# Optimization experiments

Measured on AMD Instinct MI355X. Metric: run time of the kernel, lower is better.

## Reference

```python
import jax, jax.numpy as jnp
import numpy as np

N = 100000
E = 1600000
IN_CH = 128
HID = 128
HEADS = 4
C = HID // HEADS  # 32 per-head channels
NUM_CLASSES = 40
NEG_SLOPE = 0.2


def _glorot(key, shape):
    fan_in, fan_out = shape[0], shape[-1]
    lim = jnp.sqrt(6.0 / (fan_in + fan_out))
    return jax.random.uniform(key, shape, jnp.float32, -lim, lim)


def setup_inputs() -> dict:
    key = jax.random.key(0)
    ks = jax.random.split(key, 12)
    x = jax.random.normal(ks[0], (N, IN_CH), jnp.float32)
    edge_index = jax.random.randint(ks[1], (2, E), 0, N, jnp.int64)
    edge_weight = jax.random.uniform(ks[2], (E,), jnp.float32)
    return {
        'x': x,
        'edge_index': edge_index,
        'edge_weight': edge_weight,
        'W_pre': _glorot(ks[3], (IN_CH, HID)),
        'Wl': _glorot(ks[4], (HID, HEADS * C)),
        'bl': jnp.zeros((HEADS * C,), jnp.float32),
        'Wr': _glorot(ks[5], (HID, HEADS * C)),
        'br': jnp.zeros((HEADS * C,), jnp.float32),
        'We': _glorot(ks[6], (1, HEADS * C)),
        'att': _glorot(ks[7], (HEADS, C)),
        'b_gat': jnp.zeros((HEADS * C,), jnp.float32),
        'W1': _glorot(ks[8], (HID, HID)),
        'b1': jnp.zeros((HID,), jnp.float32),
        'W2': _glorot(ks[9], (HID, NUM_CLASSES)),
        'b2': jnp.zeros((NUM_CLASSES,), jnp.float32),
    }


def reference(x, edge_index, edge_weight, W_pre, Wl, bl, Wr, br, We, att, b_gat, W1, b1, W2, b2):
    # pre projection (bias=False), norm = Identity
    h0 = x @ W_pre  # [N, HID]

    # --- GATv2Conv (PyG semantics, eval mode) ---
    # add self loops; self-loop edge_attr = mean of existing edge_attr (fill_value='mean')
    loop = jnp.arange(N, dtype=edge_index.dtype)
    src = jnp.concatenate([edge_index[0], loop])  # [E+N]
    dst = jnp.concatenate([edge_index[1], loop])
    ea = jnp.concatenate([edge_weight, jnp.full((N,), jnp.mean(edge_weight), edge_weight.dtype)])  # [E+N]

    x_l = (h0 @ Wl + bl).reshape(N, HEADS, C)  # source transform
    x_r = (h0 @ Wr + br).reshape(N, HEADS, C)  # target transform
    edge_emb = (ea[:, None] * We).reshape(-1, HEADS, C)  # lin_edge (bias=False)

    xj = x_l[src]  # [Etot, H, C] gather of source features
    e = jax.nn.leaky_relu(xj + x_r[dst] + edge_emb, NEG_SLOPE)
    alpha = jnp.einsum('ehc,hc->eh', e, att)  # [Etot, H]

    # segment softmax over destination neighborhoods
    amax = jax.ops.segment_max(alpha, dst, num_segments=N)
    amax = jnp.where(jnp.isfinite(amax), amax, 0.0)
    ex = jnp.exp(alpha - amax[dst])
    denom = jax.ops.segment_sum(ex, dst, num_segments=N)
    attn = ex / (denom[dst] + 1e-16)  # [Etot, H]

    out = jax.ops.segment_sum(attn[:, :, None] * xj, dst, num_segments=N)  # [N, H, C]
    out = out.reshape(N, HEADS * C) + b_gat

    h1 = jax.nn.elu(out)
    h = h0 + h1  # residual

    logits = jax.nn.relu(h @ W1 + b1) @ W2 + b2
    return h, logits
```

## Files before the change

### kernel.cpp

```cpp
#include <hip/hip_runtime.h>

typedef __attribute__((ext_vector_type(8))) short short8;
typedef __attribute__((ext_vector_type(16))) float f32x16;

#if __has_builtin(__builtin_amdgcn_exp2f)
#define EXP2(x) __builtin_amdgcn_exp2f(x)
#else
#define EXP2(x) exp2f(x)
#endif

static __device__ __forceinline__ unsigned short f2bf(float f){
  unsigned u = __float_as_uint(f);
  unsigned r = u + 0x7fffu + ((u >> 16) & 1u);
  return (unsigned short)(r >> 16);
}
static __device__ __forceinline__ float bf2f(unsigned short h){
  return __uint_as_float(((unsigned)h) << 16);
}

__global__ void wprep(const float* __restrict__ Wpre, const float* __restrict__ Wl,
                      const float* __restrict__ Wr, const float* __restrict__ W1,
                      const float* __restrict__ W2, const float* __restrict__ bl,
                      const float* __restrict__ br,
                      unsigned short* __restrict__ Phi, unsigned short* __restrict__ Plo,
                      unsigned short* __restrict__ Lhi, unsigned short* __restrict__ Llo,
                      unsigned short* __restrict__ W1hi, unsigned short* __restrict__ W1lo,
                      unsigned short* __restrict__ W2hi, unsigned short* __restrict__ W2lo,
                      float* __restrict__ bcat){
  int i = blockIdx.x*256 + threadIdx.x;
  float v; unsigned short* hp; unsigned short* lp; int oi;
  if (i < 16384){
    int c = i >> 7, k = i & 127;
    v = Wpre[(size_t)k*128 + c]; hp = Phi; lp = Plo; oi = i;
  } else if (i < 49152){
    int j = i - 16384; int c = j >> 7, k = j & 127;
    v = (c < 128) ? Wl[(size_t)k*128 + c] : Wr[(size_t)k*128 + (c-128)];
    hp = Lhi; lp = Llo; oi = j;
  } else if (i < 65536){
    int j = i - 49152; int c = j >> 7, k = j & 127;
    v = W1[(size_t)k*128 + c]; hp = W1hi; lp = W1lo; oi = j;
  } else if (i < 70656){
    int j = i - 65536; int c = j >> 7, k = j & 127;
    v = W2[(size_t)k*40 + c]; hp = W2hi; lp = W2lo; oi = j;
  } else if (i < 70912){
    int j = i - 70656;
    bcat[j] = (j < 128) ? bl[j] : br[j-128];
    return;
  } else return;
  unsigned short h = f2bf(v);
  hp[oi] = h;
  lp[oi] = f2bf(v - bf2f(h));
}

__global__ void count_mean(const int* __restrict__ ei, const float* __restrict__ ew,
                           int* __restrict__ deg, int* __restrict__ rk,
                           float* __restrict__ msum, int E){
  float s = 0.f;
  for (int e = blockIdx.x*256 + threadIdx.x; e < E; e += gridDim.x*256){
    rk[e] = atomicAdd(&deg[ei[E + e]], 1);
    s += ew[e];
  }
  for (int d = 32; d > 0; d >>= 1) s += __shfl_down(s, d, 64);
  __shared__ float ps[4];
  int lane = threadIdx.x & 63, w = threadIdx.x >> 6;
  if (lane == 0) ps[w] = s;
  __syncthreads();
  if (threadIdx.x == 0) atomicAdd(msum, (ps[0]+ps[1]+ps[2]+ps[3]) / (float)E);
}

__global__ __launch_bounds__(256) void scan1_kernel(const int* __restrict__ deg, int* __restrict__ rowptr,
                                                    int* __restrict__ bsum, int N){
  __shared__ int s[256];
  int i = blockIdx.x*256 + threadIdx.x;
  int v = (i < N) ? deg[i] : 0;
  s[threadIdx.x] = v;
  __syncthreads();
  for (int off = 1; off < 256; off <<= 1){
    int t = (threadIdx.x >= off) ? s[threadIdx.x - off] : 0;
    __syncthreads();
    s[threadIdx.x] += t;
    __syncthreads();
  }
  if (i < N) rowptr[i + 1] = s[threadIdx.x];
  if (threadIdx.x == 255) bsum[blockIdx.x] = s[255];
}

__global__ __launch_bounds__(512) void scan2_kernel(const int* __restrict__ bsum, int* __restrict__ boff, int nb){
  __shared__ int s[512];
  int v = (threadIdx.x < nb) ? bsum[threadIdx.x] : 0;
  s[threadIdx.x] = v;
  __syncthreads();
  for (int off = 1; off < 512; off <<= 1){
    int t = (threadIdx.x >= off) ? s[threadIdx.x - off] : 0;
    __syncthreads();
    s[threadIdx.x] += t;
    __syncthreads();
  }
  if (threadIdx.x < nb) boff[threadIdx.x] = s[threadIdx.x] - v;
}

__global__ void scan3_kernel(int* __restrict__ rowptr, const int* __restrict__ boff, int N){
  int i = blockIdx.x*256 + threadIdx.x;
  if (i == 0) rowptr[0] = 0;
  if (i < N) rowptr[i + 1] += boff[i >> 8];
}

__global__ void fill_kernel(const int* __restrict__ ei, const float* __restrict__ ew,
                            const int* __restrict__ rowptr, const int* __restrict__ rk,
                            int2* __restrict__ erec, int E){
  int e = blockIdx.x*256 + threadIdx.x;
  if (e >= E) return;
  int dst = ei[E + e];
  erec[rowptr[dst] + rk[e]] = make_int2(ei[e], __float_as_int(ew[e]));
}

template<int NT>
static __device__ __forceinline__ void stageA(short* alds, const float* __restrict__ A,
                                              int row0, int N, int t){
  for (int g = t; g < 1024; g += NT){
    int r = g >> 4, k8 = g & 15;
    int grow = row0 + r;
    float4 p0, p1;
    if (grow < N){
      const float* ap = A + (size_t)grow*128 + k8*8;
      p0 = *(const float4*)ap;
      p1 = *(const float4*)(ap + 4);
    } else {
      p0 = make_float4(0.f,0.f,0.f,0.f); p1 = p0;
    }
    float vv[8] = {p0.x,p0.y,p0.z,p0.w,p1.x,p1.y,p1.z,p1.w};
    short8 hv, lv;
    #pragma unroll
    for (int j = 0; j < 8; ++j){
      unsigned short h = f2bf(vv[j]);
      hv[j] = (short)h;
      lv[j] = (short)f2bf(vv[j] - bf2f(h));
    }
    int slot = k8 ^ (r & 15);
    *(short8*)&alds[r*128 + slot*8] = hv;
    *(short8*)&alds[8192 + r*128 + slot*8] = lv;
  }
}

#define MFMA_KLOOP(ACC0, ACC1) \
  _Pragma("unroll") \
  for (int ks = 0; ks < 8; ++ks){ \
    int k8 = ks*2 + kg; \
    const short* a0 = &alds[r0*128 + (k8 ^ sx)*8]; \
    const short* a1 = &alds[(r0+32)*128 + (k8 ^ sx)*8]; \
    short8 a0h = *(const short8*)a0; \
    short8 a0l = *(const short8*)(a0 + 8192); \
    short8 a1h = *(const short8*)a1; \
    short8 a1l = *(const short8*)(a1 + 8192); \
    ACC0 = __builtin_amdgcn_mfma_f32_32x32x16_bf16(a0h, bh[ks],  ACC0, 0,0,0); \
    ACC1 = __builtin_amdgcn_mfma_f32_32x32x16_bf16(a1h, bh[ks],  ACC1, 0,0,0); \
    ACC0 = __builtin_amdgcn_mfma_f32_32x32x16_bf16(a0l, bh[ks],  ACC0, 0,0,0); \
    ACC1 = __builtin_amdgcn_mfma_f32_32x32x16_bf16(a1l, bh[ks],  ACC1, 0,0,0); \
    ACC0 = __builtin_amdgcn_mfma_f32_32x32x16_bf16(a0h, bl8[ks], ACC0, 0,0,0); \
    ACC1 = __builtin_amdgcn_mfma_f32_32x32x16_bf16(a1h, bl8[ks], ACC1, 0,0,0); \
  }

__global__ __launch_bounds__(512) void pre_kernel(
    const float* __restrict__ A,
    const unsigned short* __restrict__ Phi, const unsigned short* __restrict__ Plo,
    const unsigned short* __restrict__ Lhi, const unsigned short* __restrict__ Llo,
    const float* __restrict__ bcat,
    float* __restrict__ hout, unsigned short* __restrict__ xlr, int N)
{
  __shared__ short alds[2*64*128];
  const int t = threadIdx.x;
  const int row0 = blockIdx.x * 64;
  stageA<512>(alds, A, row0, N, t);
  __syncthreads();

  const int lane = t & 63, w = t >> 6;
  const int cl = lane & 31, kg = lane >> 5;
  const int sx = cl & 15;

  {
    const int rt = w & 1, ct = w >> 1;
    const int colp = ct*32 + cl;
    short8 bh[8], bl8[8];
    #pragma unroll
    for (int ks = 0; ks < 8; ++ks){
      size_t off = (size_t)colp*128 + ks*16 + kg*8;
      bh[ks]  = *(const short8*)(Phi + off);
      bl8[ks] = *(const short8*)(Plo + off);
    }
    f32x16 acc;
    #pragma unroll
    for (int i = 0; i < 16; ++i) acc[i] = 0.f;
    const int r0 = rt*32 + cl;
    #pragma unroll
    for (int ks = 0; ks < 8; ++ks){
      int k8 = ks*2 + kg;
      const short* a = &alds[r0*128 + (k8 ^ sx)*8];
      short8 ah = *(const short8*)a;
      short8 al = *(const short8*)(a + 8192);
      acc = __builtin_amdgcn_mfma_f32_32x32x16_bf16(ah, bh[ks],  acc, 0,0,0);
      acc = __builtin_amdgcn_mfma_f32_32x32x16_bf16(al, bh[ks],  acc, 0,0,0);
      acc = __builtin_amdgcn_mfma_f32_32x32x16_bf16(ah, bl8[ks], acc, 0,0,0);
    }
    __syncthreads();
    #pragma unroll
    for (int reg = 0; reg < 16; ++reg){
      int row = rt*32 + (reg & 3) + 8*(reg >> 2) + 4*kg;
      float v = acc[reg];
      int grow = row0 + row;
      if (grow < N) hout[(size_t)grow*128 + colp] = v;
      unsigned short h = f2bf(v);
      unsigned short l = f2bf(v - bf2f(h));
      int idx = row*128 + (((colp >> 3) ^ (row & 15)) << 3) + (colp & 7);
      alds[idx] = (short)h;
      alds[8192 + idx] = (short)l;
    }
  }
  __syncthreads();

  {
    const int col = w*32 + cl;
    short8 bh[8], bl8[8];
    #pragma unroll
    for (int ks = 0; ks < 8; ++ks){
      size_t off = (size_t)col*128 + ks*16 + kg*8;
      bh[ks]  = *(const short8*)(Lhi + off);
      bl8[ks] = *(const short8*)(Llo + off);
    }
    f32x16 acc0, acc1;
    #pragma unroll
    for (int i = 0; i < 16; ++i){ acc0[i] = 0.f; acc1[i] = 0.f; }
    const int r0 = cl;
    MFMA_KLOOP(acc0, acc1)
    float bv = bcat[col];
    #pragma unroll
    for (int rt2 = 0; rt2 < 2; ++rt2){
      const f32x16& ac = rt2 ? acc1 : acc0;
      #pragma unroll
      for (int reg = 0; reg < 16; ++reg){
        int row = rt2*32 + (reg & 3) + 8*(reg >> 2) + 4*kg;
        int grow = row0 + row;
        if (grow < N) xlr[(size_t)grow*256 + col] = f2bf(ac[reg] + bv);
      }
    }
  }
}

__global__ __launch_bounds__(256) void mlp_kernel(
    const float* __restrict__ A,
    const unsigned short* __restrict__ B1hi, const unsigned short* __restrict__ B1lo,
    const float* __restrict__ b1,
    const unsigned short* __restrict__ B2hi, const unsigned short* __restrict__ B2lo,
    const float* __restrict__ b2,
    float* __restrict__ logits, int N)
{
  __shared__ short alds[2*64*128];
  const int t = threadIdx.x;
  const int row0 = blockIdx.x * 64;
  stageA<256>(alds, A, row0, N, t);
  __syncthreads();

  const int lane = t & 63, w = t >> 6;
  const int cl = lane & 31, kg = lane >> 5;
  const int r0 = cl;
  const int sx = r0 & 15;

  {
    const int col = w*32 + cl;
    short8 bh[8], bl8[8];
    #pragma unroll
    for (int ks = 0; ks < 8; ++ks){
      size_t off = (size_t)col*128 + ks*16 + kg*8;
      bh[ks]  = *(const short8*)(B1hi + off);
      bl8[ks] = *(const short8*)(B1lo + off);
    }
    f32x16 acc0, acc1;
    #pragma unroll
    for (int i = 0; i < 16; ++i){ acc0[i] = 0.f; acc1[i] = 0.f; }
    MFMA_KLOOP(acc0, acc1)

    float bv = b1[col];
    __syncthreads();
    #pragma unroll
    for (int rt = 0; rt < 2; ++rt){
      const f32x16& ac = rt ? acc1 : acc0;
      #pragma unroll
      for (int reg = 0; reg < 16; ++reg){
        int row = rt*32 + (reg & 3) + 8*(reg >> 2) + 4*kg;
        float v = fmaxf(ac[reg] + bv, 0.f);
        unsigned short h = f2bf(v);
        unsigned short l = f2bf(v - bf2f(h));
        int idx = row*128 + (((col >> 3) ^ (row & 15)) << 3) + (col & 7);
        alds[idx] = (short)h;
        alds[8192 + idx] = (short)l;
      }
    }
    __syncthreads();
  }

  if (w < 2){
    const int col = w*32 + cl;
    const bool cok = col < 40;
    short8 bh[8], bl8[8];
    #pragma unroll
    for (int ks = 0; ks < 8; ++ks){
      if (cok){
        size_t off = (size_t)col*128 + ks*16 + kg*8;
        bh[ks]  = *(const short8*)(B2hi + off);
        bl8[ks] = *(const short8*)(B2lo + off);
      } else {
        #pragma unroll
        for (int j = 0; j < 8; ++j){ bh[ks][j] = 0; bl8[ks][j] = 0; }
      }
    }
    f32x16 acc0, acc1;
    #pragma unroll
    for (int i = 0; i < 16; ++i){ acc0[i] = 0.f; acc1[i] = 0.f; }
    MFMA_KLOOP(acc0, acc1)

    if (cok){
      float bv = b2[col];
      #pragma unroll
      for (int rt = 0; rt < 2; ++rt){
        const f32x16& ac = rt ? acc1 : acc0;
        #pragma unroll
        for (int reg = 0; reg < 16; ++reg){
          int row = rt*32 + (reg & 3) + 8*(reg >> 2) + 4*kg;
          int grow = row0 + row;
          if (grow < N) logits[(size_t)grow*40 + col] = ac[reg] + bv;
        }
      }
    }
  }
}

__global__ __launch_bounds__(256) void gather_kernel(
    const int* __restrict__ rowptr, const int2* __restrict__ erec,
    const unsigned short* __restrict__ xlr,
    const float* __restrict__ We, const float* __restrict__ att,
    const float* __restrict__ msum, const float* __restrict__ bgat,
    float* __restrict__ hbuf, int N)
{
  const int wid  = threadIdx.x >> 6;
  const int lane = threadIdx.x & 63;
  const int g    = lane >> 4;
  const int l    = lane & 15;
  const int ch0  = l * 8;
  const int n    = (blockIdx.x*4 + wid)*4 + g;
  const bool nok = n < N;

  float xrv[8], wev[8], at6[8], at4[8];
  {
    short8 q = (short8)0;
    if (nok) q = *(const short8*)&xlr[(size_t)n*256 + 128 + ch0];
    float4 w0 = *(const float4*)&We[ch0];
    float4 w1 = *(const float4*)&We[ch0+4];
    float4 a0 = *(const float4*)&att[ch0];
    float4 a1 = *(const float4*)&att[ch0+4];
    const float L2E = 1.4426950408889634f;
    float wv[8] = {w0.x,w0.y,w0.z,w0.w,w1.x,w1.y,w1.z,w1.w};
    float av[8] = {a0.x,a0.y,a0.z,a0.w,a1.x,a1.y,a1.z,a1.w};
    #pragma unroll
    for (int j = 0; j < 8; ++j){
      xrv[j] = bf2f((unsigned short)q[j]);
      wev[j] = wv[j];
      at6[j] = av[j]*0.6f*L2E;
      at4[j] = av[j]*0.4f*L2E;
    }
  }

  float num[8];
  #pragma unroll
  for (int j = 0; j < 8; ++j) num[j] = 0.f;
  float den = 0.f;

  const float wm = msum[0];
  int beg = 0, end = 0;
  if (nok){ beg = rowptr[n]; end = rowptr[n + 1]; }
  const int cnt = nok ? (end - beg + 1) : 0;

  int itMax = cnt;
  itMax = max(itMax, __shfl_xor(itMax, 16, 64));
  itMax = max(itMax, __shfl_xor(itMax, 32, 64));

  const int2 selfrec = make_int2(nok ? n : 0, __float_as_int(wm));
  int pos = beg;
  int2 rec = (nok && beg < end) ? erec[beg] : selfrec;

  for (int it = 0; it < itMax; ++it){
    int np = pos + 1;
    int2 recN = (np < end) ? erec[np] : selfrec;

    const bool act = it < cnt;
    short8 pv = *(const short8*)&xlr[(size_t)rec.x*256 + ch0];
    const float wj = __int_as_float(rec.y);

    float xlv[8];
    #pragma unroll
    for (int q = 0; q < 8; ++q) xlv[q] = bf2f((unsigned short)pv[q]);

    float p = 0.f;
    #pragma unroll
    for (int q = 0; q < 8; ++q){
      float z = fmaf(wj, wev[q], xlv[q] + xrv[q]);
      p = fmaf(at6[q], z, p);
      p = fmaf(at4[q], fabsf(z), p);
    }
    p += __shfl_xor(p, 1, 64);
    p += __shfl_xor(p, 2, 64);
    float ex = act ? EXP2(p) : 0.f;
    den += ex;
    #pragma unroll
    for (int q = 0; q < 8; ++q) num[q] = fmaf(ex, xlv[q], num[q]);

    rec = recN; pos = np;
  }

  if (nok){
    float inv = 1.f / (den + 1e-16f);
    float o[8];
    #pragma unroll
    for (int j = 0; j < 8; ++j){
      float v = num[j]*inv + bgat[ch0+j];
      o[j] = v > 0.f ? v : expm1f(v);
    }
    float4 h0a = *(const float4*)&hbuf[(size_t)n*128 + ch0];
    float4 h0b = *(const float4*)&hbuf[(size_t)n*128 + ch0 + 4];
    h0a.x += o[0]; h0a.y += o[1]; h0a.z += o[2]; h0a.w += o[3];
    h0b.x += o[4]; h0b.y += o[5]; h0b.z += o[6]; h0b.w += o[7];
    *(float4*)&hbuf[(size_t)n*128 + ch0]     = h0a;
    *(float4*)&hbuf[(size_t)n*128 + ch0 + 4] = h0b;
  }
}

extern "C" void kernel_launch(void* const* d_in, const int* in_sizes, int n_in,
                              void* d_out, int out_size, void* d_ws, size_t ws_size,
                              hipStream_t stream)
{
  const float* x    = (const float*)d_in[0];
  const int*   ei   = (const int*)  d_in[1];
  const float* ew   = (const float*)d_in[2];
  const float* Wpre = (const float*)d_in[3];
  const float* Wl   = (const float*)d_in[4];
  const float* bl   = (const float*)d_in[5];
  const float* Wr   = (const float*)d_in[6];
  const float* br   = (const float*)d_in[7];
  const float* We   = (const float*)d_in[8];
  const float* att  = (const float*)d_in[9];
  const float* bgat = (const float*)d_in[10];
  const float* W1   = (const float*)d_in[11];
  const float* b1   = (const float*)d_in[12];
  const float* W2   = (const float*)d_in[13];
  const float* b2   = (const float*)d_in[14];

  const int N = in_sizes[0] / 128;
  const int E = in_sizes[2];
  const int nb = (N + 255) / 256;

  float* hout   = (float*)d_out;
  float* logits = hout + (size_t)N*128;

  unsigned short* xlr = (unsigned short*)d_ws;
  int2*  erec   = (int2*)(xlr + (size_t)N*256);
  int*   rk     = (int*)(erec + E);
  int*   rowptr = rk + E;
  int*   cursor = rowptr + N + 1;
  float* msum   = (float*)(cursor + N);
  int*   bsum   = (int*)(msum + 1);
  int*   boff   = bsum + nb;
  float* bcat   = (float*)(boff + nb);
  unsigned short* wsp = (unsigned short*)(((uintptr_t)(bcat + 256) + 15) & ~(uintptr_t)15);
  unsigned short* Phi  = wsp;
  unsigned short* Plo  = Phi + 16384;
  unsigned short* Lhi  = Plo + 16384;
  unsigned short* Llo  = Lhi + 32768;
  unsigned short* W1hi = Llo + 32768;
  unsigned short* W1lo = W1hi + 16384;
  unsigned short* W2hi = W1lo + 16384;
  unsigned short* W2lo = W2hi + 5120;

  hipMemsetAsync(cursor, 0, (size_t)(N + 1) * sizeof(int), stream);

  wprep<<<278, 256, 0, stream>>>(Wpre, Wl, Wr, W1, W2, bl, br,
                                 Phi, Plo, Lhi, Llo, W1hi, W1lo, W2hi, W2lo, bcat);
  count_mean<<<1024, 256, 0, stream>>>(ei, ew, cursor, rk, msum, E);
  scan1_kernel<<<nb, 256, 0, stream>>>(cursor, rowptr, bsum, N);
  scan2_kernel<<<1, 512, 0, stream>>>(bsum, boff, nb);
  scan3_kernel<<<nb, 256, 0, stream>>>(rowptr, boff, N);
  fill_kernel<<<(E + 255)/256, 256, 0, stream>>>(ei, ew, rowptr, rk, erec, E);

  const int gg = (N + 63) / 64;
  pre_kernel<<<gg, 512, 0, stream>>>(x, Phi, Plo, Lhi, Llo, bcat, hout, xlr, N);

  gather_kernel<<<(N + 15)/16, 256, 0, stream>>>(rowptr, erec, xlr, We, att, msum, bgat, hout, N);

  mlp_kernel<<<gg, 256, 0, stream>>>(hout, W1hi, W1lo, b1, W2hi, W2lo, b2, logits, N);
}
```

Measured before the change: 341.2 us.

## Sort nodes by degree for gather load balance and deepen gather prefetch

Builds a degree histogram in the scan kernels and a counting-sort permutation of nodes by in-degree, so the gather kernel processes nodes with similar degree together in each wavefront. This cuts idle lanes caused by the per-wave max-iteration loop. It also deepens the gather loop's software pipeline to prefetch two edge records and their source feature rows ahead. In exchange, it adds atomics to the scan kernels, an extra perm indirection, scattered output writes, and some register pressure.

```diff
diff --git a/kernel.cpp b/kernel.cpp
--- a/kernel.cpp
+++ b/kernel.cpp
@@ -69,10 +69,11 @@
 }
 
 __global__ __launch_bounds__(256) void scan1_kernel(const int* __restrict__ deg, int* __restrict__ rowptr,
-                                                    int* __restrict__ bsum, int N){
+                                                    int* __restrict__ bsum, int* __restrict__ dhist, int N){
   __shared__ int s[256];
   int i = blockIdx.x*256 + threadIdx.x;
   int v = (i < N) ? deg[i] : 0;
+  if (i < N) atomicAdd(&dhist[v < 255 ? v : 255], 1);
   s[threadIdx.x] = v;
   __syncthreads();
   for (int off = 1; off < 256; off <<= 1){
@@ -85,8 +86,10 @@
   if (threadIdx.x == 255) bsum[blockIdx.x] = s[255];
 }
 
-__global__ __launch_bounds__(512) void scan2_kernel(const int* __restrict__ bsum, int* __restrict__ boff, int nb){
+__global__ __launch_bounds__(512) void scan2_kernel(const int* __restrict__ bsum, int* __restrict__ boff, int nb,
+                                                    const int* __restrict__ dhist, int* __restrict__ dhoff){
   __shared__ int s[512];
+  __shared__ int s2[256];
   int v = (threadIdx.x < nb) ? bsum[threadIdx.x] : 0;
   s[threadIdx.x] = v;
   __syncthreads();
@@ -97,12 +100,30 @@
     __syncthreads();
   }
   if (threadIdx.x < nb) boff[threadIdx.x] = s[threadIdx.x] - v;
-}
-
-__global__ void scan3_kernel(int* __restrict__ rowptr, const int* __restrict__ boff, int N){
+  int v2 = 0;
+  if (threadIdx.x < 256){ v2 = dhist[threadIdx.x]; s2[threadIdx.x] = v2; }
+  __syncthreads();
+  for (int off = 1; off < 256; off <<= 1){
+    int t = 0;
+    if (threadIdx.x < 256 && threadIdx.x >= off) t = s2[threadIdx.x - off];
+    __syncthreads();
+    if (threadIdx.x < 256) s2[threadIdx.x] += t;
+    __syncthreads();
+  }
+  if (threadIdx.x < 256) dhoff[threadIdx.x] = s2[threadIdx.x] - v2;
+}
+
+__global__ void scan3_kernel(int* __restrict__ rowptr, const int* __restrict__ boff,
+                             const int* __restrict__ deg, int* __restrict__ dhoff,
+                             int* __restrict__ perm, int N){
   int i = blockIdx.x*256 + threadIdx.x;
   if (i == 0) rowptr[0] = 0;
-  if (i < N) rowptr[i + 1] += boff[i >> 8];
+  if (i < N){
+    rowptr[i + 1] += boff[i >> 8];
+    int d = deg[i]; d = d < 255 ? d : 255;
+    int pos = atomicAdd(&dhoff[d], 1);
+    perm[pos] = i;
+  }
 }
 
 __global__ void fill_kernel(const int* __restrict__ ei, const float* __restrict__ ew,
@@ -336,6 +357,7 @@
 __global__ __launch_bounds__(256) void gather_kernel(
     const int* __restrict__ rowptr, const int2* __restrict__ erec,
     const unsigned short* __restrict__ xlr,
+    const int* __restrict__ perm,
     const float* __restrict__ We, const float* __restrict__ att,
     const float* __restrict__ msum, const float* __restrict__ bgat,
     float* __restrict__ hbuf, int N)
@@ -345,13 +367,13 @@
   const int g    = lane >> 4;
   const int l    = lane & 15;
   const int ch0  = l * 8;
-  const int n    = (blockIdx.x*4 + wid)*4 + g;
-  const bool nok = n < N;
+  const int slot = (blockIdx.x*4 + wid)*4 + g;
+  const bool nok = slot < N;
+  const int n    = nok ? perm[slot] : 0;
 
   float xrv[8], wev[8], at6[8], at4[8];
   {
-    short8 q = (short8)0;
-    if (nok) q = *(const short8*)&xlr[(size_t)n*256 + 128 + ch0];
+    short8 q = *(const short8*)&xlr[(size_t)n*256 + 128 + ch0];
     float4 w0 = *(const float4*)&We[ch0];
     float4 w1 = *(const float4*)&We[ch0+4];
     float4 a0 = *(const float4*)&att[ch0];
@@ -382,21 +404,24 @@
   itMax = max(itMax, __shfl_xor(itMax, 16, 64));
   itMax = max(itMax, __shfl_xor(itMax, 32, 64));
 
-  const int2 selfrec = make_int2(nok ? n : 0, __float_as_int(wm));
+  const int2 selfrec = make_int2(n, __float_as_int(wm));
+
   int pos = beg;
-  int2 rec = (nok && beg < end) ? erec[beg] : selfrec;
+  int2 rec0 = (pos     < end) ? erec[pos]     : selfrec;
+  int2 rec1 = (pos + 1 < end) ? erec[pos + 1] : selfrec;
+  short8 pv0 = *(const short8*)&xlr[(size_t)rec0.x*256 + ch0];
+  short8 pv1 = *(const short8*)&xlr[(size_t)rec1.x*256 + ch0];
 
   for (int it = 0; it < itMax; ++it){
-    int np = pos + 1;
-    int2 recN = (np < end) ? erec[np] : selfrec;
+    int2 rec2 = (pos + 2 < end) ? erec[pos + 2] : selfrec;
+    short8 pv2 = *(const short8*)&xlr[(size_t)rec2.x*256 + ch0];
 
     const bool act = it < cnt;
-    short8 pv = *(const short8*)&xlr[(size_t)rec.x*256 + ch0];
-    const float wj = __int_as_float(rec.y);
+    const float wj = __int_as_float(rec0.y);
 
     float xlv[8];
     #pragma unroll
-    for (int q = 0; q < 8; ++q) xlv[q] = bf2f((unsigned short)pv[q]);
+    for (int q = 0; q < 8; ++q) xlv[q] = bf2f((unsigned short)pv0[q]);
 
     float p = 0.f;
     #pragma unroll
@@ -412,7 +437,9 @@
     #pragma unroll
     for (int q = 0; q < 8; ++q) num[q] = fmaf(ex, xlv[q], num[q]);
 
-    rec = recN; pos = np;
+    rec0 = rec1; rec1 = rec2;
+    pv0 = pv1;  pv1 = pv2;
+    ++pos;
   }
 
   if (nok){
@@ -465,9 +492,12 @@
   int*   rowptr = rk + E;
   int*   cursor = rowptr + N + 1;
   float* msum   = (float*)(cursor + N);
-  int*   bsum   = (int*)(msum + 1);
+  int*   dhist  = (int*)(msum + 1);
+  int*   bsum   = dhist + 256;
   int*   boff   = bsum + nb;
-  float* bcat   = (float*)(boff + nb);
+  int*   dhoff  = boff + nb;
+  int*   perm   = dhoff + 256;
+  float* bcat   = (float*)(perm + N);
   unsigned short* wsp = (unsigned short*)(((uintptr_t)(bcat + 256) + 15) & ~(uintptr_t)15);
   unsigned short* Phi  = wsp;
   unsigned short* Plo  = Phi + 16384;
@@ -478,20 +508,20 @@
   unsigned short* W2hi = W1lo + 16384;
   unsigned short* W2lo = W2hi + 5120;
 
-  hipMemsetAsync(cursor, 0, (size_t)(N + 1) * sizeof(int), stream);
+  hipMemsetAsync(cursor, 0, (size_t)(N + 1 + 256) * sizeof(int), stream);
 
   wprep<<<278, 256, 0, stream>>>(Wpre, Wl, Wr, W1, W2, bl, br,
                                  Phi, Plo, Lhi, Llo, W1hi, W1lo, W2hi, W2lo, bcat);
   count_mean<<<1024, 256, 0, stream>>>(ei, ew, cursor, rk, msum, E);
-  scan1_kernel<<<nb, 256, 0, stream>>>(cursor, rowptr, bsum, N);
-  scan2_kernel<<<1, 512, 0, stream>>>(bsum, boff, nb);
-  scan3_kernel<<<nb, 256, 0, stream>>>(rowptr, boff, N);
+  scan1_kernel<<<nb, 256, 0, stream>>>(cursor, rowptr, bsum, dhist, N);
+  scan2_kernel<<<1, 512, 0, stream>>>(bsum, boff, nb, dhist, dhoff);
+  scan3_kernel<<<nb, 256, 0, stream>>>(rowptr, boff, cursor, dhoff, perm, N);
   fill_kernel<<<(E + 255)/256, 256, 0, stream>>>(ei, ew, rowptr, rk, erec, E);
 
   const int gg = (N + 63) / 64;
   pre_kernel<<<gg, 512, 0, stream>>>(x, Phi, Plo, Lhi, Llo, bcat, hout, xlr, N);
 
-  gather_kernel<<<(N + 15)/16, 256, 0, stream>>>(rowptr, erec, xlr, We, att, msum, bgat, hout, N);
+  gather_kernel<<<(N + 15)/16, 256, 0, stream>>>(rowptr, erec, xlr, perm, We, att, msum, bgat, hout, N);
 
   mlp_kernel<<<gg, 256, 0, stream>>>(hout, W1hi, W1lo, b1, W2hi, W2lo, b2, logits, N);
 }
```

Result: slower. 805.5 us (+136.1%).
